# Performance work log

Hardware: AMD Instinct MI355X
Metric: run time of the kernel (lower is better)

## Reference

```python
import jax, jax.numpy as jnp
import numpy as np

N, E, D_IN, D, HEADS = 8192, 2048, 256, 256, 4
EPS = 1e-5
NEG = -1e9  # large negative instead of -inf (rows guaranteed non-empty anyway)


def _layernorm(x, g, b):
    mu = jnp.mean(x, axis=-1, keepdims=True)
    var = jnp.mean(jnp.square(x - mu), axis=-1, keepdims=True)
    return (x - mu) * jax.lax.rsqrt(var + EPS) * g + b


def _mha(q_x, kv_x, in_w, in_b, out_w, out_b, mask):
    """torch nn.MultiheadAttention (batch=1, eval) with boolean attn_mask.
    q_x: [Lq, D], kv_x: [Lk, D], mask: [Lq, Lk] True = blocked."""
    hd = D // HEADS
    wq, wk, wv = jnp.split(in_w, 3, axis=0)   # each [D, D]
    bq, bk, bv = jnp.split(in_b, 3, axis=0)
    q = (q_x @ wq.T + bq).reshape(-1, HEADS, hd).transpose(1, 0, 2)  # [h, Lq, hd]
    k = (kv_x @ wk.T + bk).reshape(-1, HEADS, hd).transpose(1, 0, 2)
    v = (kv_x @ wv.T + bv).reshape(-1, HEADS, hd).transpose(1, 0, 2)
    scores = jnp.einsum('hqd,hkd->hqk', q, k) / jnp.sqrt(jnp.asarray(hd, q.dtype))
    scores = jnp.where(mask[None, :, :], NEG, scores)
    attn = jax.nn.softmax(scores, axis=-1)
    out = jnp.einsum('hqk,hkd->hqd', attn, v)           # [h, Lq, hd]
    out = out.transpose(1, 0, 2).reshape(-1, D)          # [Lq, D]
    return out @ out_w.T + out_b


def setup_inputs() -> dict:
    key = jax.random.key(0)
    ks = jax.random.split(key, 12)
    s = 0.02
    x_0 = jax.random.normal(ks[0], (N, D_IN), jnp.float32)
    x_1 = jax.random.normal(ks[1], (E, D_IN), jnp.float32)
    H = (jax.random.uniform(ks[2], (N, E)) < 0.01).astype(jnp.float32)
    H = H.at[jnp.arange(N), jnp.arange(N) % E].set(1.0)
    return {
        'x_0': x_0, 'x_1': x_1, 'incidence_1': H,
        'node_w': jax.random.normal(ks[3], (D, D_IN), jnp.float32) * s,
        'node_b': jnp.zeros((D,), jnp.float32),
        'edge_w': jax.random.normal(ks[4], (D, D_IN), jnp.float32) * s,
        'edge_b': jnp.zeros((D,), jnp.float32),
        'n2e_in_w': jax.random.normal(ks[5], (3 * D, D), jnp.float32) * s,
        'n2e_in_b': jnp.zeros((3 * D,), jnp.float32),
        'n2e_out_w': jax.random.normal(ks[6], (D, D), jnp.float32) * s,
        'n2e_out_b': jnp.zeros((D,), jnp.float32),
        'e2n_in_w': jax.random.normal(ks[7], (3 * D, D), jnp.float32) * s,
        'e2n_in_b': jnp.zeros((3 * D,), jnp.float32),
        'e2n_out_w': jax.random.normal(ks[8], (D, D), jnp.float32) * s,
        'e2n_out_b': jnp.zeros((D,), jnp.float32),
        'norm1_g': jnp.ones((D,), jnp.float32),
        'norm1_b': jnp.zeros((D,), jnp.float32),
        'norm2_g': jnp.ones((D,), jnp.float32),
        'norm2_b': jnp.zeros((D,), jnp.float32),
    }


def reference(x_0, x_1, incidence_1, node_w, node_b, edge_w, edge_b,
              n2e_in_w, n2e_in_b, n2e_out_w, n2e_out_b,
              e2n_in_w, e2n_in_b, e2n_out_w, e2n_out_b,
              norm1_g, norm1_b, norm2_g, norm2_b):
    H = incidence_1                      # [N, E]
    x_0_p = x_0 @ node_w.T + node_b      # [N, D]
    x_1_p = x_1 @ edge_w.T + edge_b      # [E, D]
    # node -> edge: edges query nodes, mask where H.T == 0
    x_1_u = _mha(x_1_p, x_0_p, n2e_in_w, n2e_in_b, n2e_out_w, n2e_out_b,
                 H.T == 0)
    x_1_u = _layernorm(x_1_p + x_1_u, norm1_g, norm1_b)
    # edge -> node: nodes query updated edges, mask where H == 0
    x_0_u = _mha(x_0_p, x_1_u, e2n_in_w, e2n_in_b, e2n_out_w, e2n_out_b,
                 H == 0)
    x_0_u = _layernorm(x_0_p + x_0_u, norm2_g, norm2_b)
    return (x_0_u, x_1_u)
```

## Files before the change

### kernel.cpp

```cpp
#include <hip/hip_runtime.h>
#include <hip/hip_bf16.h>

using bf16 = __hip_bfloat16;
typedef __attribute__((ext_vector_type(4))) float  f32x4;
typedef __attribute__((ext_vector_type(8))) short  s16x8;

#define QSTRIDE 1040
#define ASTRIDE 520
#define BSTRIDE 2064
#define CMAX 256
#define RMAX 128
#define CSTRIDE 16

#define O_MW0  0
#define O_MB0  262144
#define O_MW1  263168
#define O_MB1  394240
#define O_KV2W 394752
#define O_KV2B 525824
#define O_O1W  526336
#define O_O2W  591872

struct PrepDesc {
    const float* aw[4]; const float* pw[4];
    const float* ab[4]; const float* pb[4];
    int cdst[4]; int bdst[4];
    const float* csrc[8]; int coff[8]; int ccnt[8];
};

__global__ __launch_bounds__(256)
void prep_front(PrepDesc d, bf16* __restrict__ dst,
                const float* __restrict__ H, int* __restrict__ col_cnt,
                int* __restrict__ row_cnt, unsigned short* __restrict__ row_idx)
{
    const int t = threadIdx.x;

    if (blockIdx.x >= 256) {
        const int b = blockIdx.x - 256;
        if (t < 16) col_cnt[b * 16 + t] = 0;

        const int lane = t & 63;
        const int n = b * 4 + (t >> 6);
        const unsigned long long ltm = (1ull << lane) - 1ull;
        int base = 0;

#pragma unroll
        for (int seg = 0; seg < 8; seg++) {
            f32x4 v = *(const f32x4*)(H + (size_t)n * 2048 + seg * 256 + lane * 4);
            unsigned long long bm[4];
#pragma unroll
            for (int j = 0; j < 4; j++) bm[j] = __ballot(v[j] != 0.f);

            int pre = 0;
#pragma unroll
            for (int j = 0; j < 4; j++) {
                if (v[j] != 0.f) {
                    const int slot = base + pre + (int)__popcll(bm[j] & ltm);
                    if (slot < RMAX)
                        row_idx[(size_t)n * RMAX + slot] =
                            (unsigned short)(seg * 256 + lane * 4 + j);
                }
                pre += (int)__popcll(bm[j]);
            }
            base += pre;
        }
        if (lane == 0) row_cnt[n] = (base < RMAX) ? base : RMAX;
        return;
    }

    if (blockIdx.x < 128) {
        const int combo = blockIdx.x >> 5;
        const int i0    = (blockIdx.x & 31) * 8;
        const float* __restrict__ Aw = d.aw[combo];
        const float* __restrict__ Bw = d.pw[combo];

        float acc[8];
#pragma unroll
        for (int i = 0; i < 8; i++) acc[i] = 0.f;

#pragma unroll 4
        for (int k = 0; k < 256; k++) {
            const float bv = Bw[k * 256 + t];
#pragma unroll
            for (int i = 0; i < 8; i++)
                acc[i] += Aw[(i0 + i) * 256 + k] * bv;
        }
        bf16* o = dst + d.cdst[combo];
#pragma unroll
        for (int i = 0; i < 8; i++)
            o[(i0 + i) * 256 + t] = __float2bfloat16(acc[i]);

        {
            const int i  = t >> 5;
            const int kk = (t & 31) * 8;
            float s = 0.f;
#pragma unroll
            for (int u = 0; u < 8; u++)
                s += Aw[(i0 + i) * 256 + kk + u] * d.pb[combo][kk + u];
#pragma unroll
            for (int o2 = 1; o2 < 32; o2 <<= 1) s += __shfl_xor(s, o2);
            if ((t & 31) == 0)
                dst[d.bdst[combo] + i0 + i] =
                    __float2bfloat16(d.ab[combo][i0 + i] + s);
        }
        return;
    }

    const int seg = (blockIdx.x - 128) >> 4;
    const int blk = (blockIdx.x - 128) & 15;
    const float* __restrict__ s = d.csrc[seg];
    bf16* __restrict__ o = dst + d.coff[seg];
    const int n = d.ccnt[seg];
    for (int i = blk * 256 + t; i < n; i += 16 * 256)
        o[i] = __float2bfloat16(s[i]);
}

__global__ __launch_bounds__(256, 2)
void gemm_mega(const float* __restrict__ X0, const float* __restrict__ X1,
               const bf16* __restrict__ wc,
               bf16* __restrict__ x0cat, bf16* __restrict__ x1cat,
               const int* __restrict__ row_cnt,
               const unsigned short* __restrict__ row_idx,
               int* __restrict__ col_cnt, unsigned short* __restrict__ col_idx)
{
    __shared__ __align__(16) bf16 As[4 * QSTRIDE];
    __shared__ __align__(16) bf16 Bs[4 * QSTRIDE];

    const int t = threadIdx.x;

    if (blockIdx.x >= 576) {
        const int g = (blockIdx.x - 576) * 256 + t;
        const int n = g >> 3;
        const int tt = g & 7;
        const int cnt = row_cnt[n];
        for (int i = tt; i < cnt; i += 8) {
            const int e = row_idx[(size_t)n * RMAX + i];
            const int s = atomicAdd(&col_cnt[e * CSTRIDE], 1);
            if (s < CMAX) col_idx[(size_t)e * CMAX + s] = (unsigned short)n;
        }
        return;
    }

    const int lane = t & 63;
    const int w    = t >> 6;
    const int wm   = (w >> 1) * 64;
    const int wn   = (w & 1) * 64;

    int rt, ct, ostride;
    const float* __restrict__ A;
    const bf16* __restrict__ W;
    const bf16* __restrict__ bias;
    bf16* __restrict__ outp;
    if (blockIdx.x < 512) {
        rt = blockIdx.x >> 3; ct = blockIdx.x & 7;
        A = X0; W = wc + O_MW0; bias = wc + O_MB0; outp = x0cat; ostride = 1024;
    } else {
        const int b = blockIdx.x - 512;
        rt = b >> 2; ct = b & 3;
        A = X1; W = wc + O_MW1; bias = wc + O_MB1; outp = x1cat; ostride = 512;
    }
    const int arow = rt * 128;
    const int tn   = ct * 128;

    f32x4 acc[4][4];
#pragma unroll
    for (int i = 0; i < 4; i++)
#pragma unroll
        for (int j = 0; j < 4; j++)
#pragma unroll
            for (int r = 0; r < 4; r++) acc[i][j][r] = 0.f;

    const int m0 = t >> 2,         q0 = t & 3;
    const int m1 = (t + 256) >> 2, q1 = (t + 256) & 3;
    const int fq = lane >> 4, fr = lane & 15;

    for (int k0 = 0; k0 < 256; k0 += 32) {
        f32x4 a0l = *(const f32x4*)(A + (size_t)(arow + m0) * 256 + k0 + q0 * 8);
        f32x4 a0h = *(const f32x4*)(A + (size_t)(arow + m0) * 256 + k0 + q0 * 8 + 4);
        f32x4 a1l = *(const f32x4*)(A + (size_t)(arow + m1) * 256 + k0 + q1 * 8);
        f32x4 a1h = *(const f32x4*)(A + (size_t)(arow + m1) * 256 + k0 + q1 * 8 + 4);
        union { s16x8 v; bf16 e[8]; } u0, u1;
#pragma unroll
        for (int j = 0; j < 4; j++) {
            u0.e[j] = __float2bfloat16(a0l[j]); u0.e[4 + j] = __float2bfloat16(a0h[j]);
            u1.e[j] = __float2bfloat16(a1l[j]); u1.e[4 + j] = __float2bfloat16(a1h[j]);
        }
        s16x8 sb0 = *(const s16x8*)(W + (size_t)(tn + m0) * 256 + k0 + q0 * 8);
        s16x8 sb1 = *(const s16x8*)(W + (size_t)(tn + m1) * 256 + k0 + q1 * 8);

        __syncthreads();
        *(s16x8*)&As[q0 * QSTRIDE + m0 * 8] = u0.v;
        *(s16x8*)&As[q1 * QSTRIDE + m1 * 8] = u1.v;
        *(s16x8*)&Bs[q0 * QSTRIDE + m0 * 8] = sb0;
        *(s16x8*)&Bs[q1 * QSTRIDE + m1 * 8] = sb1;
        __syncthreads();

        s16x8 af[4], bfv[4];
#pragma unroll
        for (int i = 0; i < 4; i++) {
            af[i]  = *(const s16x8*)&As[fq * QSTRIDE + (wm + i * 16 + fr) * 8];
            bfv[i] = *(const s16x8*)&Bs[fq * QSTRIDE + (wn + i * 16 + fr) * 8];
        }
#pragma unroll
        for (int i = 0; i < 4; i++)
#pragma unroll
            for (int j = 0; j < 4; j++)
                acc[i][j] = __builtin_amdgcn_mfma_f32_16x16x32_bf16(
                    af[i], bfv[j], acc[i][j], 0, 0, 0);
    }

#pragma unroll
    for (int j = 0; j < 4; j++) {
        const int ncol = tn + wn + j * 16 + fr;
        const float bj = __bfloat162float(bias[ncol]);
#pragma unroll
        for (int i = 0; i < 4; i++)
#pragma unroll
            for (int r = 0; r < 4; r++) {
                const int mrow = arow + wm + i * 16 + fq * 4 + r;
                outp[(size_t)mrow * ostride + ncol] = __float2bfloat16(acc[i][j][r] + bj);
            }
    }
}

__global__ __launch_bounds__(256, 2)
void gemm_dual(const bf16* __restrict__ A0, const bf16* __restrict__ W0,
               const bf16* __restrict__ bias0, bf16* __restrict__ out0,
               int N0, int tiles0, int nblk0,
               const bf16* __restrict__ A1, const bf16* __restrict__ W1,
               const bf16* __restrict__ bias1, bf16* __restrict__ out1,
               int N1, int tiles1)
{
    __shared__ __align__(16) bf16 As[4 * QSTRIDE];
    __shared__ __align__(16) bf16 Bs[4 * QSTRIDE];

    const int t    = threadIdx.x;
    const int lane = t & 63;
    const int w    = t >> 6;
    const int wm   = (w >> 1) * 64;
    const int wn   = (w & 1) * 64;

    const bool second = (blockIdx.x >= (unsigned)nblk0);
    const int  bi     = second ? (blockIdx.x - nblk0) : blockIdx.x;
    const bf16* __restrict__ A    = second ? A1 : A0;
    const bf16* __restrict__ W    = second ? W1 : W0;
    const bf16* __restrict__ bias = second ? bias1 : bias0;
    bf16* __restrict__ outB       = second ? out1 : out0;
    const int N      = second ? N1 : N0;
    const int tilesN = second ? tiles1 : tiles0;
    const int tm = (bi / tilesN) * 128;
    const int tn = (bi % tilesN) * 128;

    f32x4 acc[4][4];
#pragma unroll
    for (int i = 0; i < 4; i++)
#pragma unroll
        for (int j = 0; j < 4; j++)
#pragma unroll
            for (int r = 0; r < 4; r++) acc[i][j][r] = 0.f;

    const int m0 = t >> 2,         q0 = t & 3;
    const int m1 = (t + 256) >> 2, q1 = (t + 256) & 3;
    const int fq = lane >> 4, fr = lane & 15;

    for (int k0 = 0; k0 < 256; k0 += 32) {
        s16x8 sa0 = *(const s16x8*)(A + (size_t)(tm + m0) * 256 + k0 + q0 * 8);
        s16x8 sa1 = *(const s16x8*)(A + (size_t)(tm + m1) * 256 + k0 + q1 * 8);
        s16x8 sb0 = *(const s16x8*)(W + (size_t)(tn + m0) * 256 + k0 + q0 * 8);
        s16x8 sb1 = *(const s16x8*)(W + (size_t)(tn + m1) * 256 + k0 + q1 * 8);

        __syncthreads();
        *(s16x8*)&As[q0 * QSTRIDE + m0 * 8] = sa0;
        *(s16x8*)&As[q1 * QSTRIDE + m1 * 8] = sa1;
        *(s16x8*)&Bs[q0 * QSTRIDE + m0 * 8] = sb0;
        *(s16x8*)&Bs[q1 * QSTRIDE + m1 * 8] = sb1;
        __syncthreads();

        s16x8 af[4], bfv[4];
#pragma unroll
        for (int i = 0; i < 4; i++) {
            af[i]  = *(const s16x8*)&As[fq * QSTRIDE + (wm + i * 16 + fr) * 8];
            bfv[i] = *(const s16x8*)&Bs[fq * QSTRIDE + (wn + i * 16 + fr) * 8];
        }
#pragma unroll
        for (int i = 0; i < 4; i++)
#pragma unroll
            for (int j = 0; j < 4; j++)
                acc[i][j] = __builtin_amdgcn_mfma_f32_16x16x32_bf16(
                    af[i], bfv[j], acc[i][j], 0, 0, 0);
    }

#pragma unroll
    for (int j = 0; j < 4; j++) {
        const int ncol = tn + wn + j * 16 + fr;
        const float bj = __bfloat162float(bias[ncol]);
#pragma unroll
        for (int i = 0; i < 4; i++)
#pragma unroll
            for (int r = 0; r < 4; r++) {
                const int mrow = tm + wm + i * 16 + fq * 4 + r;
                outB[(size_t)mrow * N + ncol] = __float2bfloat16(acc[i][j][r] + bj);
            }
    }
}

__global__ __launch_bounds__(256, 2)
void gemm_ln(const bf16* __restrict__ A, const bf16* __restrict__ W,
             const float* __restrict__ biasF, const bf16* __restrict__ xp, int xps,
             const float* __restrict__ g, const float* __restrict__ b,
             float* __restrict__ outF, bf16* __restrict__ outB)
{
    __shared__ __align__(16) bf16 As[4 * ASTRIDE];
    __shared__ __align__(16) bf16 Bs[4 * BSTRIDE];
    __shared__ float rs1[64], rs2[64];

    const int t    = threadIdx.x;
    const int lane = t & 63;
    const int w    = t >> 6;
    const int fq   = lane >> 4;
    const int fr   = lane & 15;
    const int tm   = blockIdx.x * 64;

    if (t < 64) { rs1[t] = 0.f; rs2[t] = 0.f; }

    f32x4 acc[4][4];
#pragma unroll
    for (int i = 0; i < 4; i++)
#pragma unroll
        for (int j = 0; j < 4; j++)
#pragma unroll
            for (int r = 0; r < 4; r++) acc[i][j][r] = 0.f;

    const int mA = t >> 2, qA = t & 3;

    for (int k0 = 0; k0 < 256; k0 += 32) {
        s16x8 sa = *(const s16x8*)(A + (size_t)(tm + mA) * 256 + k0 + qA * 8);
        s16x8 sb[4];
#pragma unroll
        for (int s = 0; s < 4; s++)
            sb[s] = *(const s16x8*)(W + (size_t)(mA + 64 * s) * 256 + k0 + qA * 8);

        __syncthreads();
        *(s16x8*)&As[qA * ASTRIDE + mA * 8] = sa;
#pragma unroll
        for (int s = 0; s < 4; s++)
            *(s16x8*)&Bs[qA * BSTRIDE + (mA + 64 * s) * 8] = sb[s];
        __syncthreads();

        s16x8 af[4], bfv[4];
#pragma unroll
        for (int i = 0; i < 4; i++) {
            af[i]  = *(const s16x8*)&As[fq * ASTRIDE + (i * 16 + fr) * 8];
            bfv[i] = *(const s16x8*)&Bs[fq * BSTRIDE + (w * 64 + i * 16 + fr) * 8];
        }
#pragma unroll
        for (int i = 0; i < 4; i++)
#pragma unroll
            for (int j = 0; j < 4; j++)
                acc[i][j] = __builtin_amdgcn_mfma_f32_16x16x32_bf16(
                    af[i], bfv[j], acc[i][j], 0, 0, 0);
    }

    float bj[4], gj[4], bbj[4];
    int colv[4];
#pragma unroll
    for (int j = 0; j < 4; j++) {
        colv[j] = w * 64 + j * 16 + fr;
        bj[j]  = biasF[colv[j]];
        gj[j]  = g[colv[j]];
        bbj[j] = b[colv[j]];
    }

#pragma unroll
    for (int i = 0; i < 4; i++) {
#pragma unroll
        for (int r = 0; r < 4; r++) {
            const int row = i * 16 + fq * 4 + r;
            float t1 = 0.f, t2 = 0.f;
#pragma unroll
            for (int j = 0; j < 4; j++) {
                float v = acc[i][j][r] + bj[j]
                        + __bfloat162float(xp[(size_t)(tm + row) * xps + colv[j]]);
                acc[i][j][r] = v;
                t1 += v;
                t2 += v * v;
            }
#pragma unroll
            for (int o = 1; o < 16; o <<= 1) {
                t1 += __shfl_xor(t1, o);
                t2 += __shfl_xor(t2, o);
            }
            if (fr == 0) {
                atomicAdd(&rs1[row], t1);
                atomicAdd(&rs2[row], t2);
            }
        }
    }
    __syncthreads();

#pragma unroll
    for (int i = 0; i < 4; i++) {
#pragma unroll
        for (int r = 0; r < 4; r++) {
            const int row = i * 16 + fq * 4 + r;
            const float mu  = rs1[row] * (1.f / 256.f);
            const float var = rs2[row] * (1.f / 256.f) - mu * mu;
            const float rstd = rsqrtf(var + 1e-5f);
#pragma unroll
            for (int j = 0; j < 4; j++) {
                const float y = (acc[i][j][r] - mu) * rstd * gj[j] + bbj[j];
                outF[(size_t)(tm + row) * 256 + colv[j]] = y;
                if (outB) outB[(size_t)(tm + row) * 256 + colv[j]] = __float2bfloat16(y);
            }
        }
    }
}

__global__ __launch_bounds__(256)
void sparse_attn(const bf16* __restrict__ Q, int qs,
                 const bf16* __restrict__ Kb, const bf16* __restrict__ Vb, int kvs,
                 const int* __restrict__ cnts, int cstride,
                 const unsigned short* __restrict__ idx,
                 int lmax, int idxmask, bf16* __restrict__ out)
{
    __shared__ float sc[4][CMAX];
    __shared__ unsigned short nls[CMAX];
    const int qi   = blockIdx.x;
    const int h    = threadIdx.x >> 6;
    const int lane = threadIdx.x & 63;
    const int grp  = lane >> 3;
    const int sub  = lane & 7;

    int n = cnts[(size_t)qi * cstride];
    if (n > lmax) n = lmax;

    if (h == 0)
        for (int i = lane; i < n; i += 64)
            nls[i] = (unsigned short)(((int)idx[(size_t)qi * lmax + i]) & idxmask);
    __syncthreads();

    if (n <= 0) {
        out[(size_t)qi * 256 + h * 64 + lane] = __float2bfloat16(0.f);
        return;
    }

    float qv[8];
    {
        union { f32x4 v; unsigned short u[8]; } qu;
        qu.v = *(const f32x4*)(Q + (size_t)qi * qs + h * 64 + sub * 8);
#pragma unroll
        for (int j = 0; j < 8; j++)
            qv[j] = __uint_as_float(((unsigned)qu.u[j]) << 16) * 0.125f;
    }

    float mx = -1e30f;
#pragma unroll 2
    for (int base = 0; base < n; base += 8) {
        const int i = base + grp;
        float s = -1e30f;
        if (i < n) {
            const int nb = nls[i];
            union { f32x4 v; unsigned short u[8]; } ku;
            ku.v = *(const f32x4*)(Kb + (size_t)nb * kvs + h * 64 + sub * 8);
            float a = 0.f;
#pragma unroll
            for (int j = 0; j < 8; j++)
                a += __uint_as_float(((unsigned)ku.u[j]) << 16) * qv[j];
            a += __shfl_xor(a, 1);
            a += __shfl_xor(a, 2);
            a += __shfl_xor(a, 4);
            if (sub == 0) sc[h][i] = a;
            s = a;
        }
        mx = fmaxf(mx, s);
    }
#pragma unroll
    for (int o = 32; o > 0; o >>= 1) mx = fmaxf(mx, __shfl_xor(mx, o));

    float sum = 0.f;
    for (int base = 0; base < n; base += 64) {
        const int i = base + lane;
        if (i < n) {
            const float p = __expf(sc[h][i] - mx);
            sc[h][i] = p;
            sum += p;
        }
    }
#pragma unroll
    for (int o = 32; o > 0; o >>= 1) sum += __shfl_xor(sum, o);
    const float inv = 1.f / sum;

    float oa[8];
#pragma unroll
    for (int j = 0; j < 8; j++) oa[j] = 0.f;
#pragma unroll 2
    for (int base = 0; base < n; base += 8) {
        const int i = base + grp;
        if (i < n) {
            const float p = sc[h][i];
            const int nb = nls[i];
            union { f32x4 v; unsigned short u[8]; } vu;
            vu.v = *(const f32x4*)(Vb + (size_t)nb * kvs + h * 64 + sub * 8);
#pragma unroll
            for (int j = 0; j < 8; j++)
                oa[j] += p * __uint_as_float(((unsigned)vu.u[j]) << 16);
        }
    }
#pragma unroll
    for (int j = 0; j < 8; j++) {
        oa[j] += __shfl_xor(oa[j], 8);
        oa[j] += __shfl_xor(oa[j], 16);
        oa[j] += __shfl_xor(oa[j], 32);
    }
    if (grp == 0) {
        union { s16x8 v; bf16 e[8]; } ou;
#pragma unroll
        for (int j = 0; j < 8; j++) ou.e[j] = __float2bfloat16(oa[j] * inv);
        *(s16x8*)(out + (size_t)qi * 256 + h * 64 + sub * 8) = ou.v;
    }
}

extern "C" void kernel_launch(void* const* d_in, const int* in_sizes, int n_in,
                              void* d_out, int out_size, void* d_ws, size_t ws_size,
                              hipStream_t stream)
{
    const int N = 8192, E = 2048;

    float* out0 = (float*)d_out;
    float* out1 = (float*)d_out + (size_t)N * 256;

    char* wp = (char*)d_ws;
    auto carve = [&](size_t bytes) { void* p = wp; wp += (bytes + 15) & ~size_t(15); return p; };

    bf16*  wcat    = (bf16*)          carve(657408 * 2);
    int*   col_cnt = (int*)           carve((size_t)E * CSTRIDE * 4);
    int*   row_cnt = (int*)           carve((size_t)N * 4);
    unsigned short* col_idx = (unsigned short*)carve((size_t)E * CMAX * 2);
    unsigned short* row_idx = (unsigned short*)carve((size_t)N * RMAX * 2);
    bf16*  x0cat   = (bf16*) carve((size_t)N * 1024 * 2);
    bf16*  x1cat   = (bf16*) carve((size_t)E * 512 * 2);
    bf16*  attn1   = (bf16*) carve((size_t)E * 256 * 2);
    bf16*  x1u_b   = (bf16*) carve((size_t)E * 256 * 2);
    bf16*  kv2     = (bf16*) carve((size_t)E * 512 * 2);
    bf16*  attn2   = (bf16*) carve((size_t)N * 256 * 2);

    const float* nw = (const float*)d_in[3];
    const float* nb = (const float*)d_in[4];
    const float* ew = (const float*)d_in[5];
    const float* eb = (const float*)d_in[6];
    const float* w1 = (const float*)d_in[7];
    const float* b1 = (const float*)d_in[8];
    const float* w2 = (const float*)d_in[11];
    const float* b2 = (const float*)d_in[12];

    PrepDesc pd;
    pd.aw[0] = w1 + 65536;  pd.pw[0] = nw; pd.ab[0] = b1 + 256; pd.pb[0] = nb;
    pd.cdst[0] = O_MW0 + 65536;  pd.bdst[0] = O_MB0 + 256;
    pd.aw[1] = w1 + 131072; pd.pw[1] = nw; pd.ab[1] = b1 + 512; pd.pb[1] = nb;
    pd.cdst[1] = O_MW0 + 131072; pd.bdst[1] = O_MB0 + 512;
    pd.aw[2] = w2;          pd.pw[2] = nw; pd.ab[2] = b2;      pd.pb[2] = nb;
    pd.cdst[2] = O_MW0 + 196608; pd.bdst[2] = O_MB0 + 768;
    pd.aw[3] = w1;          pd.pw[3] = ew; pd.ab[3] = b1;      pd.pb[3] = eb;
    pd.cdst[3] = O_MW1 + 65536;  pd.bdst[3] = O_MB1 + 256;
    const float* csrc[8] = { nw, ew, w2 + 65536, (const float*)d_in[9],
                             (const float*)d_in[13], nb, eb, b2 + 256 };
    const int coff[8] = {O_MW0, O_MW1, O_KV2W, O_O1W, O_O2W, O_MB0, O_MB1, O_KV2B};
    const int ccnt[8] = {65536, 65536, 131072, 65536, 65536, 256, 256, 512};
    for (int i = 0; i < 8; i++) { pd.csrc[i] = csrc[i]; pd.coff[i] = coff[i]; pd.ccnt[i] = ccnt[i]; }

    prep_front<<<256 + 2048, 256, 0, stream>>>(pd, wcat, (const float*)d_in[2],
                                               col_cnt, row_cnt, row_idx);

    gemm_mega<<<576 + 256, 256, 0, stream>>>((const float*)d_in[0],
                                             (const float*)d_in[1], wcat,
                                             x0cat, x1cat,
                                             row_cnt, row_idx, col_cnt, col_idx);

    sparse_attn<<<E, 256, 0, stream>>>(x1cat + 256, 512,
                                       x0cat + 256, x0cat + 512, 1024,
                                       col_cnt, CSTRIDE, col_idx, CMAX, N - 1, attn1);
    gemm_ln<<<E / 64, 256, 0, stream>>>(attn1, wcat + O_O1W, (const float*)d_in[10],
                                        x1cat, 512,
                                        (const float*)d_in[15], (const float*)d_in[16],
                                        out1, x1u_b);

    gemm_dual<<<64, 256, 0, stream>>>(x1u_b, wcat + O_KV2W, wcat + O_KV2B, kv2,
                                      512, 4, 64,
                                      nullptr, nullptr, nullptr, nullptr, 256, 2);
    sparse_attn<<<N, 256, 0, stream>>>(x0cat + 768, 1024, kv2, kv2 + 256, 512,
                                       row_cnt, 1, row_idx, RMAX, E - 1, attn2);
    gemm_ln<<<N / 64, 256, 0, stream>>>(attn2, wcat + O_O2W, (const float*)d_in[14],
                                        x0cat, 1024,
                                        (const float*)d_in[17], (const float*)d_in[18],
                                        out0, nullptr);
}
```

Measured before the change: 263.4 us.

## Fuse K/V projection into first gemm_ln and stage weight rows in LDS

Removes the separate gemm_dual launch and the bf16 x1u intermediate buffer. The layernormed tile is kept in shared memory and each gemm_ln block for edges multiplies it by the K/V weights directly, reading those weights from global memory. The prep weight-combination blocks now copy their 8 A-weight rows into shared memory and unroll the k loop further. The cost is more LDS per gemm_ln block (a 32 KB Ys array), the occupancy hint of 2 is dropped, and only 32 blocks do the fused K/V work instead of 64.

```diff
diff --git a/kernel.cpp b/kernel.cpp
--- a/kernel.cpp
+++ b/kernel.cpp
@@ -8,6 +8,7 @@
 #define QSTRIDE 1040
 #define ASTRIDE 520
 #define BSTRIDE 2064
+#define YSTRIDE 520
 #define CMAX 256
 #define RMAX 128
 #define CSTRIDE 16
@@ -33,6 +34,7 @@
                 const float* __restrict__ H, int* __restrict__ col_cnt,
                 int* __restrict__ row_cnt, unsigned short* __restrict__ row_idx)
 {
+    __shared__ float aws[2048];
     const int t = threadIdx.x;
 
     if (blockIdx.x >= 256) {
@@ -74,16 +76,21 @@
         const float* __restrict__ Aw = d.aw[combo];
         const float* __restrict__ Bw = d.pw[combo];
 
+#pragma unroll
+        for (int i = 0; i < 8; i++)
+            aws[i * 256 + t] = Aw[(size_t)(i0 + i) * 256 + t];
+        __syncthreads();
+
         float acc[8];
 #pragma unroll
         for (int i = 0; i < 8; i++) acc[i] = 0.f;
 
-#pragma unroll 4
+#pragma unroll 16
         for (int k = 0; k < 256; k++) {
             const float bv = Bw[k * 256 + t];
 #pragma unroll
             for (int i = 0; i < 8; i++)
-                acc[i] += Aw[(i0 + i) * 256 + k] * bv;
+                acc[i] += aws[i * 256 + k] * bv;
         }
         bf16* o = dst + d.cdst[combo];
 #pragma unroll
@@ -96,7 +103,7 @@
             float s = 0.f;
 #pragma unroll
             for (int u = 0; u < 8; u++)
-                s += Aw[(i0 + i) * 256 + kk + u] * d.pb[combo][kk + u];
+                s += aws[i * 256 + kk + u] * d.pb[combo][kk + u];
 #pragma unroll
             for (int o2 = 1; o2 < 32; o2 <<= 1) s += __shfl_xor(s, o2);
             if ((t & 31) == 0)
@@ -223,95 +230,17 @@
     }
 }
 
-__global__ __launch_bounds__(256, 2)
-void gemm_dual(const bf16* __restrict__ A0, const bf16* __restrict__ W0,
-               const bf16* __restrict__ bias0, bf16* __restrict__ out0,
-               int N0, int tiles0, int nblk0,
-               const bf16* __restrict__ A1, const bf16* __restrict__ W1,
-               const bf16* __restrict__ bias1, bf16* __restrict__ out1,
-               int N1, int tiles1)
-{
-    __shared__ __align__(16) bf16 As[4 * QSTRIDE];
-    __shared__ __align__(16) bf16 Bs[4 * QSTRIDE];
-
-    const int t    = threadIdx.x;
-    const int lane = t & 63;
-    const int w    = t >> 6;
-    const int wm   = (w >> 1) * 64;
-    const int wn   = (w & 1) * 64;
-
-    const bool second = (blockIdx.x >= (unsigned)nblk0);
-    const int  bi     = second ? (blockIdx.x - nblk0) : blockIdx.x;
-    const bf16* __restrict__ A    = second ? A1 : A0;
-    const bf16* __restrict__ W    = second ? W1 : W0;
-    const bf16* __restrict__ bias = second ? bias1 : bias0;
-    bf16* __restrict__ outB       = second ? out1 : out0;
-    const int N      = second ? N1 : N0;
-    const int tilesN = second ? tiles1 : tiles0;
-    const int tm = (bi / tilesN) * 128;
-    const int tn = (bi % tilesN) * 128;
-
-    f32x4 acc[4][4];
-#pragma unroll
-    for (int i = 0; i < 4; i++)
-#pragma unroll
-        for (int j = 0; j < 4; j++)
-#pragma unroll
-            for (int r = 0; r < 4; r++) acc[i][j][r] = 0.f;
-
-    const int m0 = t >> 2,         q0 = t & 3;
-    const int m1 = (t + 256) >> 2, q1 = (t + 256) & 3;
-    const int fq = lane >> 4, fr = lane & 15;
-
-    for (int k0 = 0; k0 < 256; k0 += 32) {
-        s16x8 sa0 = *(const s16x8*)(A + (size_t)(tm + m0) * 256 + k0 + q0 * 8);
-        s16x8 sa1 = *(const s16x8*)(A + (size_t)(tm + m1) * 256 + k0 + q1 * 8);
-        s16x8 sb0 = *(const s16x8*)(W + (size_t)(tn + m0) * 256 + k0 + q0 * 8);
-        s16x8 sb1 = *(const s16x8*)(W + (size_t)(tn + m1) * 256 + k0 + q1 * 8);
-
-        __syncthreads();
-        *(s16x8*)&As[q0 * QSTRIDE + m0 * 8] = sa0;
-        *(s16x8*)&As[q1 * QSTRIDE + m1 * 8] = sa1;
-        *(s16x8*)&Bs[q0 * QSTRIDE + m0 * 8] = sb0;
-        *(s16x8*)&Bs[q1 * QSTRIDE + m1 * 8] = sb1;
-        __syncthreads();
-
-        s16x8 af[4], bfv[4];
-#pragma unroll
-        for (int i = 0; i < 4; i++) {
-            af[i]  = *(const s16x8*)&As[fq * QSTRIDE + (wm + i * 16 + fr) * 8];
-            bfv[i] = *(const s16x8*)&Bs[fq * QSTRIDE + (wn + i * 16 + fr) * 8];
-        }
-#pragma unroll
-        for (int i = 0; i < 4; i++)
-#pragma unroll
-            for (int j = 0; j < 4; j++)
-                acc[i][j] = __builtin_amdgcn_mfma_f32_16x16x32_bf16(
-                    af[i], bfv[j], acc[i][j], 0, 0, 0);
-    }
-
-#pragma unroll
-    for (int j = 0; j < 4; j++) {
-        const int ncol = tn + wn + j * 16 + fr;
-        const float bj = __bfloat162float(bias[ncol]);
-#pragma unroll
-        for (int i = 0; i < 4; i++)
-#pragma unroll
-            for (int r = 0; r < 4; r++) {
-                const int mrow = tm + wm + i * 16 + fq * 4 + r;
-                outB[(size_t)mrow * N + ncol] = __float2bfloat16(acc[i][j][r] + bj);
-            }
-    }
-}
-
-__global__ __launch_bounds__(256, 2)
+__global__ __launch_bounds__(256)
 void gemm_ln(const bf16* __restrict__ A, const bf16* __restrict__ W,
              const float* __restrict__ biasF, const bf16* __restrict__ xp, int xps,
              const float* __restrict__ g, const float* __restrict__ b,
-             float* __restrict__ outF, bf16* __restrict__ outB)
+             float* __restrict__ outF,
+             const bf16* __restrict__ W2, const bf16* __restrict__ bias2,
+             bf16* __restrict__ kvout)
 {
     __shared__ __align__(16) bf16 As[4 * ASTRIDE];
     __shared__ __align__(16) bf16 Bs[4 * BSTRIDE];
+    __shared__ __align__(16) bf16 Ys[32 * YSTRIDE];
     __shared__ float rs1[64], rs2[64];
 
     const int t    = threadIdx.x;
@@ -410,8 +339,56 @@
             for (int j = 0; j < 4; j++) {
                 const float y = (acc[i][j][r] - mu) * rstd * gj[j] + bbj[j];
                 outF[(size_t)(tm + row) * 256 + colv[j]] = y;
-                if (outB) outB[(size_t)(tm + row) * 256 + colv[j]] = __float2bfloat16(y);
+                if (kvout) {
+                    const int c = colv[j];
+                    Ys[(c >> 3) * YSTRIDE + row * 8 + (c & 7)] = __float2bfloat16(y);
+                }
             }
+        }
+    }
+
+    if (!kvout) return;
+
+    __syncthreads();
+    const int wc0 = w * 128;
+#pragma unroll
+    for (int chunk = 0; chunk < 2; chunk++) {
+        const int cbase = wc0 + chunk * 64;
+        f32x4 a2[4][4];
+#pragma unroll
+        for (int i = 0; i < 4; i++)
+#pragma unroll
+            for (int j = 0; j < 4; j++)
+#pragma unroll
+                for (int r = 0; r < 4; r++) a2[i][j][r] = 0.f;
+
+        for (int k0 = 0; k0 < 256; k0 += 32) {
+            s16x8 af[4], bv[4];
+#pragma unroll
+            for (int i = 0; i < 4; i++)
+                af[i] = *(const s16x8*)&Ys[(k0 / 8 + fq) * YSTRIDE + (i * 16 + fr) * 8];
+#pragma unroll
+            for (int j = 0; j < 4; j++)
+                bv[j] = *(const s16x8*)(W2 + (size_t)(cbase + j * 16 + fr) * 256 + k0 + fq * 8);
+#pragma unroll
+            for (int i = 0; i < 4; i++)
+#pragma unroll
+                for (int j = 0; j < 4; j++)
+                    a2[i][j] = __builtin_amdgcn_mfma_f32_16x16x32_bf16(
+                        af[i], bv[j], a2[i][j], 0, 0, 0);
+        }
+
+#pragma unroll
+        for (int j = 0; j < 4; j++) {
+            const int col = cbase + j * 16 + fr;
+            const float bb = __bfloat162float(bias2[col]);
+#pragma unroll
+            for (int i = 0; i < 4; i++)
+#pragma unroll
+                for (int r = 0; r < 4; r++) {
+                    const int row = i * 16 + fq * 4 + r;
+                    kvout[(size_t)(tm + row) * 512 + col] = __float2bfloat16(a2[i][j][r] + bb);
+                }
         }
     }
 }
@@ -540,7 +517,6 @@
     bf16*  x0cat   = (bf16*) carve((size_t)N * 1024 * 2);
     bf16*  x1cat   = (bf16*) carve((size_t)E * 512 * 2);
     bf16*  attn1   = (bf16*) carve((size_t)E * 256 * 2);
-    bf16*  x1u_b   = (bf16*) carve((size_t)E * 256 * 2);
     bf16*  kv2     = (bf16*) carve((size_t)E * 512 * 2);
     bf16*  attn2   = (bf16*) carve((size_t)N * 256 * 2);
 
@@ -582,15 +558,14 @@
     gemm_ln<<<E / 64, 256, 0, stream>>>(attn1, wcat + O_O1W, (const float*)d_in[10],
                                         x1cat, 512,
                                         (const float*)d_in[15], (const float*)d_in[16],
-                                        out1, x1u_b);
-
-    gemm_dual<<<64, 256, 0, stream>>>(x1u_b, wcat + O_KV2W, wcat + O_KV2B, kv2,
-                                      512, 4, 64,
-                                      nullptr, nullptr, nullptr, nullptr, 256, 2);
+                                        out1,
+                                        wcat + O_KV2W, wcat + O_KV2B, kv2);
+
     sparse_attn<<<N, 256, 0, stream>>>(x0cat + 768, 1024, kv2, kv2 + 256, 512,
                                        row_cnt, 1, row_idx, RMAX, E - 1, attn2);
     gemm_ln<<<N / 64, 256, 0, stream>>>(attn2, wcat + O_O2W, (const float*)d_in[14],
                                         x0cat, 1024,
                                         (const float*)d_in[17], (const float*)d_in[18],
-                                        out0, nullptr);
+                                        out0,
+                                        nullptr, nullptr, nullptr);
 }
```

Result: faster. 255.8 us (-2.9%).
